# Kernel optimization log

Hardware: AMD Instinct MI355X
Metric: run time of the kernel (lower is better)

## Reference

```python
import jax, jax.numpy as jnp
import numpy as np
from jax import lax

B, T, U, V = 4, 256, 64, 1024   # batch, enc frames, max target len, vocab (blank=0)
F, H, HD, J = 80, 512, 512, 512  # feat dim, enc dim, dec dim, joint dim
NEG = -1e30


def setup_inputs() -> dict:
    key = jax.random.key(0)
    ks = jax.random.split(key, 10)
    inputs = jax.random.normal(ks[0], (B, T, F), dtype=jnp.float32)
    targets = jax.random.randint(ks[1], (B, U), 1, V, dtype=jnp.int32)  # labels exclude blank=0
    input_lengths = jax.random.randint(ks[2], (B,), T // 2, T + 1, dtype=jnp.int32)
    target_lengths = jax.random.randint(ks[3], (B,), U // 2, U + 1, dtype=jnp.int32)
    s = 0.02
    W_enc = jax.random.normal(ks[4], (F, H), dtype=jnp.float32) * s
    emb = jax.random.normal(ks[5], (V, HD), dtype=jnp.float32) * s
    W_jenc = jax.random.normal(ks[6], (H, J), dtype=jnp.float32) * s
    W_jdec = jax.random.normal(ks[7], (HD, J), dtype=jnp.float32) * s
    b_j = jnp.zeros((J,), dtype=jnp.float32)
    W_out = jax.random.normal(ks[8], (J, V), dtype=jnp.float32) * s
    b_out = jnp.zeros((V,), dtype=jnp.float32)
    return {"inputs": inputs, "W_enc": W_enc, "emb": emb, "W_jenc": W_jenc,
            "W_jdec": W_jdec, "b_j": b_j, "W_out": W_out, "b_out": b_out,
            "targets": targets, "input_lengths": input_lengths,
            "target_lengths": target_lengths}


def rnnt_loss(log_probs, targets, in_lens, tgt_lens):
    """RNN-T loss (blank=0, 'gather' variant: gather blank/label lps, then DP).
    log_probs: (B,T,U+1,V) log-softmaxed joint. Returns mean loss over batch."""
    Bq, Tq, U1, _ = log_probs.shape
    Uq = U1 - 1
    blank_lp = log_probs[..., 0]                                    # (B,T,U+1)
    lbl_lp = jnp.take_along_axis(
        log_probs[:, :, :Uq, :],
        jnp.broadcast_to(targets[:, None, :, None], (Bq, Tq, Uq, 1)),
        axis=3)[..., 0]                                             # (B,T,U)
    u_idx = jnp.arange(Uq)
    lbl_lp = jnp.where(u_idx[None, None, :] < tgt_lens[:, None, None], lbl_lp, NEG)

    def row(a, py):
        # a: (B,U+1) = alpha_prev + blank emission; py: (B,U) label lps this frame
        def step(c, x):
            a_u, py_prev = x
            c = jnp.logaddexp(a_u, c + py_prev)
            return c, c
        c0 = a[:, 0]
        _, rest = lax.scan(step, c0, (a[:, 1:].T, py.T))            # (U,B)
        return jnp.concatenate([c0[:, None], rest.T], axis=1)      # (B,U+1)

    # t=0 row: alpha[0,u] = cumsum of label lps at frame 0
    alpha0 = jnp.concatenate(
        [jnp.zeros((Bq, 1), log_probs.dtype),
         jnp.cumsum(lbl_lp[:, 0, :], axis=1)], axis=1)              # (B,U+1)

    def tstep(alpha_prev, x):
        blank_prev, py_t = x
        alpha = row(alpha_prev + blank_prev, py_t)
        return alpha, alpha

    xs = (jnp.swapaxes(blank_lp[:, :-1, :], 0, 1),                  # (T-1,B,U+1)
          jnp.swapaxes(lbl_lp[:, 1:, :], 0, 1))                    # (T-1,B,U)
    _, rest = lax.scan(tstep, alpha0, xs)
    alphas = jnp.concatenate([alpha0[None], rest], axis=0)          # (T,B,U+1)

    b = jnp.arange(Bq)
    t_last = in_lens - 1
    a_fin = alphas[t_last, b, tgt_lens] + blank_lp[b, t_last, tgt_lens]
    return -jnp.mean(a_fin)


def reference(inputs, W_enc, emb, W_jenc, W_jdec, b_j, W_out, b_out,
              targets, input_lengths, target_lengths):
    enc = inputs @ W_enc                                            # (B,T,H) encoder
    padded = jnp.concatenate(
        [jnp.zeros((targets.shape[0], 1), targets.dtype), targets], axis=1)
    dec = emb[padded]                                               # (B,U+1,HD) decoder
    e = enc @ W_jenc                                                # (B,T,J)
    d = dec @ W_jdec                                                # (B,U+1,J)
    h = jnp.tanh(e[:, :, None, :] + d[:, None, :, :] + b_j)        # (B,T,U+1,J)
    logits = h @ W_out + b_out                                      # (B,T,U+1,V)
    log_probs = jax.nn.log_softmax(logits, axis=-1)
    return rnnt_loss(log_probs, targets, input_lengths, target_lengths)
```

## Files before the change

### kernel.cpp

```cpp
#include <hip/hip_runtime.h>
#include <stdint.h>

#define NEGF (-1e30f)

typedef unsigned short ushort_t;
typedef unsigned char uchar_t;
typedef __attribute__((ext_vector_type(2))) long v2i64;
typedef __attribute__((ext_vector_type(4))) float f32x4;

constexpr int cB = 4, cT = 256, cU = 64, cU1 = 65, cV = 1024, cF = 80, cH = 512, cJ = 512;
constexpr int cM = cB * cT * cU1;
constexpr int cTU = cT * cU1;

__device__ __forceinline__ float tanh_fast(float x){
  float t = x * x;
  float num = x * (27.f + t);
  float den = fmaf(9.f, t, 27.f);
  float r = num * __builtin_amdgcn_rcpf(den);
  return fminf(1.f, fmaxf(-1.f, r));
}

__device__ __forceinline__ float logadd(float x, float y){
  float m = fmaxf(x, y);
  return m + __logf(1.f + __expf(-fabsf(x - y)));
}

__device__ __forceinline__ int pk8(float a, float b, float c, float d){
  int v = __builtin_amdgcn_cvt_pk_fp8_f32(a, b, 0, false);
  v = __builtin_amdgcn_cvt_pk_fp8_f32(c, d, v, true);
  return v;
}

__global__ __launch_bounds__(256) void k_pre(
    const float* __restrict__ W_enc, const float* __restrict__ W_jenc,
    float* __restrict__ Wcomb,
    const float* __restrict__ emb, const int* __restrict__ targets,
    const float* __restrict__ W_jdec, const float* __restrict__ b_j,
    float* __restrict__ dmatb,
    const float* __restrict__ W_out, uchar_t* __restrict__ WTf8)
{
  __shared__ float sA[4][512];
  int bid = blockIdx.x;
  int tid = threadIdx.x;

  if (bid < 170){
    bool isW = (bid < 40);
    int id = isW ? bid : bid - 40;
    int bx = id & 1, by = id >> 1;
    int m0 = by * 4;
    int col = bx * 256 + tid;
    const float* Bm = isW ? W_jenc : W_jdec;
    for (int i = tid; i < 4 * 512; i += 256){
      int r = i >> 9, c = i & 511;
      if (isW){
        sA[r][c] = W_enc[(size_t)(m0 + r) * 512 + c];
      } else {
        int row = m0 + r;
        int b = row / cU1, u = row % cU1;
        int src = (u == 0) ? 0 : targets[b * cU + (u - 1)];
        sA[r][c] = emb[(size_t)src * cH + c];
      }
    }
    __syncthreads();
    float a0 = 0.f, a1 = 0.f, a2 = 0.f, a3 = 0.f;
#pragma unroll 8
    for (int k = 0; k < 512; k++){
      float bv = Bm[(size_t)k * cJ + col];
      a0 = fmaf(sA[0][k], bv, a0);
      a1 = fmaf(sA[1][k], bv, a1);
      a2 = fmaf(sA[2][k], bv, a2);
      a3 = fmaf(sA[3][k], bv, a3);
    }
    float bb = isW ? 0.f : b_j[col];
    float* C = isW ? Wcomb : dmatb;
    C[(size_t)(m0 + 0) * cJ + col] = a0 + bb;
    C[(size_t)(m0 + 1) * cJ + col] = a1 + bb;
    C[(size_t)(m0 + 2) * cJ + col] = a2 + bb;
    C[(size_t)(m0 + 3) * cJ + col] = a3 + bb;
  } else {
    int id = bid - 170;
    int bn = id & 3, ksp = id >> 2;
    int lane = tid & 63, nth = tid >> 6;
    int c16 = lane & 15, quad = lane >> 4;
    int jA = ksp * 64 + quad * 8;
#pragma unroll
    for (int i = 0; i < 4; i++){
      int nt16 = nth * 4 + i;
      int n = bn * 256 + nt16 * 16 + c16;
      unsigned int p[4];
#pragma unroll
      for (int h = 0; h < 4; h++){
        int j0 = jA + (h >> 1) * 32 + (h & 1) * 4;
        float w0 = W_out[(size_t)(j0 + 0) * cV + n] * 32.f;
        float w1 = W_out[(size_t)(j0 + 1) * cV + n] * 32.f;
        float w2 = W_out[(size_t)(j0 + 2) * cV + n] * 32.f;
        float w3 = W_out[(size_t)(j0 + 3) * cV + n] * 32.f;
        p[h] = (unsigned)pk8(w0, w1, w2, w3);
      }
      uint4 pack; pack.x = p[0]; pack.y = p[1]; pack.z = p[2]; pack.w = p[3];
      *(uint4*)(WTf8 + (((size_t)(bn * 8 + ksp) * 16 + nt16) * 64 + lane) * 16) = pack;
    }
  }
}

__global__ void k_gemm_e(const float* __restrict__ A, const float* __restrict__ Bm,
                         float* __restrict__ C){
  __shared__ float sA[4][80];
  int m0 = blockIdx.y * 4;
  int col = blockIdx.x * 256 + threadIdx.x;
  for (int i = threadIdx.x; i < 4 * 80; i += 256)
    sA[i / 80][i % 80] = A[(size_t)(m0 + i / 80) * 80 + (i % 80)];
  __syncthreads();
  float a0 = 0.f, a1 = 0.f, a2 = 0.f, a3 = 0.f;
#pragma unroll 8
  for (int k = 0; k < 80; k++){
    float bv = Bm[(size_t)k * cJ + col];
    a0 = fmaf(sA[0][k], bv, a0);
    a1 = fmaf(sA[1][k], bv, a1);
    a2 = fmaf(sA[2][k], bv, a2);
    a3 = fmaf(sA[3][k], bv, a3);
  }
  C[(size_t)(m0 + 0) * cJ + col] = a0;
  C[(size_t)(m0 + 1) * cJ + col] = a1;
  C[(size_t)(m0 + 2) * cJ + col] = a2;
  C[(size_t)(m0 + 3) * cJ + col] = a3;
}

__global__ __launch_bounds__(256) void k_hf(const float* __restrict__ e,
                                            const float* __restrict__ dmatb,
                                            uchar_t* __restrict__ Hbf8){
  __shared__ uchar_t sH[16 * 520];
  int tid = threadIdx.x;
  int wid = tid >> 6, lane = tid & 63;
  int c16 = lane & 15, quad = lane >> 4;
  int bm = blockIdx.x;
  int bu = bm >> 1, thalf = bm & 1;
  int b = bu / cU1;
  int t0 = thalf * 128;

  float dj[8];
  const float4* dp = (const float4*)(dmatb + (size_t)bu * cJ + lane * 8);
  float4 dA = dp[0], dB = dp[1];
  dj[0] = dA.x; dj[1] = dA.y; dj[2] = dA.z; dj[3] = dA.w;
  dj[4] = dB.x; dj[5] = dB.y; dj[6] = dB.z; dj[7] = dB.w;

  const float* erow0 = e + ((size_t)(b * cT + t0)) * cJ + lane * 8;
  uchar_t* outb = Hbf8 + (size_t)bm * 65536 + lane * 16;

  for (int mg = 0; mg < 8; mg++){
#pragma unroll
    for (int rr = 0; rr < 4; rr++){
      int rloc = wid * 4 + rr;
      const float* ep = erow0 + ((size_t)(mg * 16 + rloc)) * cJ;
      float4 e0 = *(const float4*)ep;
      float4 e1 = *(const float4*)(ep + 4);
      int v0 = pk8(tanh_fast(e0.x + dj[0]), tanh_fast(e0.y + dj[1]),
                   tanh_fast(e0.z + dj[2]), tanh_fast(e0.w + dj[3]));
      int v1 = pk8(tanh_fast(e1.x + dj[4]), tanh_fast(e1.y + dj[5]),
                   tanh_fast(e1.z + dj[6]), tanh_fast(e1.w + dj[7]));
      uint2 pk; pk.x = (unsigned)v0; pk.y = (unsigned)v1;
      *(uint2*)(sH + rloc * 520 + lane * 8) = pk;
    }
    __syncthreads();
#pragma unroll
    for (int q = 0; q < 2; q++){
      int ksp = wid * 2 + q;
      uint2 lo = *(const uint2*)(sH + c16 * 520 + ksp * 64 + quad * 8);
      uint2 hi = *(const uint2*)(sH + c16 * 520 + ksp * 64 + 32 + quad * 8);
      uint4 pack; pack.x = lo.x; pack.y = lo.y; pack.z = hi.x; pack.w = hi.y;
      *(uint4*)(outb + ((size_t)ksp * 8 + mg) * 1024) = pack;
    }
    __syncthreads();
  }
}

__global__ __launch_bounds__(256, 3) void k_joint(
    const uchar_t* __restrict__ Hbf8, const uchar_t* __restrict__ WTf8,
    const float* __restrict__ b_out, const int* __restrict__ targets,
    float* __restrict__ ps,
    float* __restrict__ blank_g, float* __restrict__ lbl_g)
{
  __shared__ float redS[2][128];

  int tid = threadIdx.x;
  int wid = tid >> 6, lane = tid & 63;
  int quad = lane >> 4, c16 = lane & 15;
  int wm = wid & 1, wn = wid >> 1;
  int bid = blockIdx.x;
  int bm = ((bid >> 6) << 3) + (bid & 7);
  int bn = (bid >> 3) & 7;
  int bu = bm >> 1, thalf = bm & 1;
  int b = bu / cU1, u = bu - b * cU1;
  int tg = (u < cU) ? targets[b * cU + u] : -1;
  int lin0 = bu * cT + thalf * 128;

  f32x4 acc[4][4];
#pragma unroll
  for (int i = 0; i < 4; i++)
#pragma unroll
    for (int j = 0; j < 4; j++)
      acc[i][j] = (f32x4){0.f, 0.f, 0.f, 0.f};

  const uchar_t* aP = Hbf8 + (size_t)bm * 65536 + (wm * 4) * 1024 + lane * 16;
  const uchar_t* bP = WTf8 + (size_t)(bn >> 1) * 131072 + ((bn & 1) * 8 + wn * 4) * 1024 + lane * 16;

#pragma unroll
  for (int ksp = 0; ksp < 8; ksp++){
    v2i64 af[4], bf[4];
#pragma unroll
    for (int mt = 0; mt < 4; mt++)
      af[mt] = *(const v2i64*)(aP + (size_t)ksp * 8192 + mt * 1024);
#pragma unroll
    for (int nt = 0; nt < 4; nt++)
      bf[nt] = *(const v2i64*)(bP + (size_t)ksp * 16384 + nt * 1024);
#pragma unroll
    for (int h = 0; h < 2; h++)
#pragma unroll
      for (int mt = 0; mt < 4; mt++)
#pragma unroll
        for (int nt = 0; nt < 4; nt++)
          acc[mt][nt] = __builtin_amdgcn_mfma_f32_16x16x32_fp8_fp8(af[mt][h], bf[nt][h], acc[mt][nt], 0, 0, 0);
  }

  float bv[4];
#pragma unroll
  for (int nt = 0; nt < 4; nt++) bv[nt] = b_out[bn * 128 + (wn * 4 + nt) * 16 + c16];

  bool ownL = (tg >= 0) && ((tg >> 7) == bn) && (((tg >> 6) & 1) == wn);
  int ntO = (tg >> 4) & 3;
  int tgc = tg & 15;
  const float descale = 1.f / 32.f;

#pragma unroll
  for (int mt = 0; mt < 4; mt++){
#pragma unroll
    for (int r = 0; r < 4; r++){
      int rl = wm * 64 + mt * 16 + quad * 4 + r;
      float l[4];
#pragma unroll
      for (int nt = 0; nt < 4; nt++) l[nt] = fmaf(acc[mt][nt][r], descale, bv[nt]);
      if (bn == 0 && wn == 0 && c16 == 0) blank_g[lin0 + rl] = l[0];
      if (ownL && c16 == tgc){
        float v = l[0];
#pragma unroll
        for (int k = 1; k < 4; k++) v = (ntO == k) ? l[k] : v;
        lbl_g[lin0 + rl] = v;
      }
      float s = __expf(l[0]) + __expf(l[1]) + __expf(l[2]) + __expf(l[3]);
      s += __shfl_xor(s, 1, 64);
      s += __shfl_xor(s, 2, 64);
      s += __shfl_xor(s, 4, 64);
      s += __shfl_xor(s, 8, 64);
      if (c16 == 0) redS[wn][rl] = s;
    }
  }
  __syncthreads();
  if (tid < 128)
    ps[(size_t)bn * cM + lin0 + tid] = redS[0][tid] + redS[1][tid];
}

__global__ __launch_bounds__(256) void k_lse(
    const float* __restrict__ ps, const float* __restrict__ blank_g,
    const float* __restrict__ lbl_g,
    float* __restrict__ blankd, float* __restrict__ lbld)
{
  int cell = blockIdx.x * 256 + threadIdx.x;
  float S = 0.f;
#pragma unroll
  for (int p = 0; p < 8; p++) S += ps[(size_t)p * cM + cell];
  float lse = __logf(S);
  int u = (cell % cTU) >> 8;
  blankd[cell] = blank_g[cell] - lse;
  lbld[cell] = (u < cU) ? (lbl_g[cell] - lse) : NEGF;
}

__global__ __launch_bounds__(256) void k_dp(
    const float* __restrict__ blankd, const float* __restrict__ lbld,
    const int* __restrict__ in_len, const int* __restrict__ tgt_len,
    float* __restrict__ afin)
{
  __shared__ float sbb[cTU];
  __shared__ float slb[cTU];
  __shared__ float sS[256];
  int b = blockIdx.x;
  int tl  = tgt_len[b];
  size_t base = (size_t)b * cTU;
  for (int i = threadIdx.x; i < cTU / 4; i += 256){
    ((float4*)sbb)[i] = ((const float4*)(blankd + base))[i];
    float4 v = ((const float4*)(lbld + base))[i];
    int row = (i * 4) >> 8;
    if (row >= tl){ v.x = NEGF; v.y = NEGF; v.z = NEGF; v.w = NEGF; }
    ((float4*)slb)[i] = v;
  }
  __syncthreads();
  if (threadIdx.x >= 64) return;

  int u = threadIdx.x;
  int til = in_len[b] - 1;
  bool cap64 = (tl == 64);
  bool isTL = (u == tl);
  const float* pbu  = sbb + (u << 8);
  const float* pbu1 = sbb + (((u >= 1) ? u - 1 : 0) << 8);
  const float* plu1 = slb + (((u >= 1) ? u - 1 : 0) << 8);
  const float* plu2 = slb + (((u >= 2) ? u - 2 : 0) << 8);
  bool u1 = (u >= 1), u2 = (u >= 2);
  float fb = pbu[til];

  float A = (u == 0) ? 0.f : NEGF;
  float res = 0.f;

  auto ld = [&](const float* p, int i, bool ok) -> float {
    bool v = ok & (i >= 0) & (i <= 255);
    int ic = (i < 0) ? 0 : ((i > 255) ? 255 : i);
    float x = p[ic];
    return v ? x : NEGF;
  };

  int i0 = -u;
  float o0 = ld(pbu,  i0,     true);
  float o1 = ld(pbu,  i0 + 1, true);
  float o2 = ld(plu1, i0 + 1, u1);
  float o3 = ld(pbu1, i0 + 1, u1);
  float o4 = ld(plu1, i0 + 2, u1);
  float o5 = ld(plu2, i0 + 2, u2);

  for (int g = 0; g < 159; g++){
    float c0 = o0, c1 = o1, c2 = o2, c3 = o3, c4 = o4, c5 = o5;
    int i0n = i0 + 2;
    o0 = ld(pbu,  i0n,     true);
    o1 = ld(pbu,  i0n + 1, true);
    o2 = ld(plu1, i0n + 1, u1);
    o3 = ld(pbu1, i0n + 1, u1);
    o4 = ld(plu1, i0n + 2, u1);
    o5 = ld(plu2, i0n + 2, u2);

    float up1 = __shfl_up(A, 1, 64);
    float up2 = __shfl_up(A, 2, 64);

    float C0 = c0 + c1;
    float C1 = logadd(c2 + c1, c3 + c4);
    float C2 = c5 + c4;

    bool tv1 = (i0 + 1 >= 0) & (i0 + 1 <= 255);
    float Amid = logadd(A + c0, up1 + c2);
    Amid = tv1 ? Amid : NEGF;
    bool tv2 = (i0 + 2 >= 0) & (i0 + 2 <= 255);
    float Anew = logadd(logadd(A + C0, up1 + C1), up2 + C2);
    Anew = tv2 ? Anew : NEGF;

    if (isTL && (i0 + 1) == til) res = Amid + fb;
    if (isTL && (i0 + 2) == til) res = Anew + fb;
    if (u == 63){
      if (tv1) sS[i0 + 1] = Amid;
      if (tv2) sS[i0 + 2] = Anew;
    }
    A = Anew;
    i0 = i0n;
  }

  if (cap64){
    const float* pb64 = sbb + (64 << 8);
    const float* pl63 = slb + (63 << 8);
    float A64 = sS[0] + pl63[0];
    for (int t = 1; t <= til; t++)
      A64 = logadd(A64 + pb64[t - 1], sS[t] + pl63[t]);
    if (u == 0) res = A64 + pb64[til];
  }

  res += __shfl_xor(res, 1, 64);
  res += __shfl_xor(res, 2, 64);
  res += __shfl_xor(res, 4, 64);
  res += __shfl_xor(res, 8, 64);
  res += __shfl_xor(res, 16, 64);
  res += __shfl_xor(res, 32, 64);
  if (u == 0) afin[b] = res;
}

__global__ void k_final(const float* __restrict__ afin, float* __restrict__ out){
  if (threadIdx.x == 0)
    out[0] = -0.25f * (afin[0] + afin[1] + afin[2] + afin[3]);
}

extern "C" void kernel_launch(void* const* d_in, const int* in_sizes, int n_in,
                              void* d_out, int out_size, void* d_ws, size_t ws_size,
                              hipStream_t stream)
{
  (void)in_sizes; (void)n_in; (void)out_size; (void)ws_size;
  const float* inputs = (const float*)d_in[0];
  const float* W_enc  = (const float*)d_in[1];
  const float* emb    = (const float*)d_in[2];
  const float* W_jenc = (const float*)d_in[3];
  const float* W_jdec = (const float*)d_in[4];
  const float* b_j    = (const float*)d_in[5];
  const float* W_out  = (const float*)d_in[6];
  const float* b_out  = (const float*)d_in[7];
  const int* targets  = (const int*)d_in[8];
  const int* in_len   = (const int*)d_in[9];
  const int* tgt_len  = (const int*)d_in[10];

  char* w = (char*)d_ws;
  auto alloc = [&](size_t bytes){ char* p = w; w += (bytes + 255) & ~(size_t)255; return p; };
  float* Wcomb   = (float*)alloc((size_t)80 * 512 * 4);
  float* e       = (float*)alloc((size_t)1024 * 512 * 4);
  float* dmatb   = (float*)alloc((size_t)260 * 512 * 4);
  float* blank_g = (float*)alloc((size_t)cM * 4);
  float* lbl_g   = (float*)alloc((size_t)cM * 4);
  float* ps      = (float*)alloc((size_t)8 * cM * 4);
  float* blankd  = (float*)alloc((size_t)cM * 4);
  float* lbld    = (float*)alloc((size_t)cM * 4);
  float* afin    = (float*)alloc(256);
  uchar_t* Hbf8  = (uchar_t*)alloc((size_t)520 * 65536);
  uchar_t* WTf8  = (uchar_t*)alloc((size_t)4 * 131072);

  k_pre<<<202, 256, 0, stream>>>(W_enc, W_jenc, Wcomb, emb, targets, W_jdec, b_j, dmatb,
                                 W_out, WTf8);
  k_gemm_e<<<dim3(2, 256), 256, 0, stream>>>(inputs, Wcomb, e);
  k_hf<<<520, 256, 0, stream>>>(e, dmatb, Hbf8);
  k_joint<<<4160, 256, 0, stream>>>(Hbf8, WTf8, b_out, targets, ps, blank_g, lbl_g);
  k_lse<<<260, 256, 0, stream>>>(ps, blank_g, lbl_g, blankd, lbld);
  k_dp<<<4, 256, 0, stream>>>(blankd, lbld, in_len, tgt_len, afin);
  k_final<<<1, 64, 0, stream>>>(afin, (float*)d_out);
}
```

Measured before the change: 244.2 us.

## Switch joint GEMM to 16x16x128 scaled FP8 MFMA with repacked operand layout

```diff
diff --git a/kernel.cpp b/kernel.cpp
--- a/kernel.cpp
+++ b/kernel.cpp
@@ -7,6 +7,7 @@
 typedef unsigned char uchar_t;
 typedef __attribute__((ext_vector_type(2))) long v2i64;
 typedef __attribute__((ext_vector_type(4))) float f32x4;
+typedef __attribute__((ext_vector_type(8))) int v8i32_t;
 
 constexpr int cB = 4, cT = 256, cU = 64, cU1 = 65, cV = 1024, cF = 80, cH = 512, cJ = 512;
 constexpr int cM = cB * cT * cU1;
@@ -79,26 +80,29 @@
     C[(size_t)(m0 + 3) * cJ + col] = a3 + bb;
   } else {
     int id = bid - 170;
-    int bn = id & 3, ksp = id >> 2;
+    int bn4 = id & 3, kq = id >> 2;
     int lane = tid & 63, nth = tid >> 6;
     int c16 = lane & 15, quad = lane >> 4;
-    int jA = ksp * 64 + quad * 8;
+    int jA = kq * 128 + quad * 32;
 #pragma unroll
     for (int i = 0; i < 4; i++){
       int nt16 = nth * 4 + i;
-      int n = bn * 256 + nt16 * 16 + c16;
-      unsigned int p[4];
-#pragma unroll
-      for (int h = 0; h < 4; h++){
-        int j0 = jA + (h >> 1) * 32 + (h & 1) * 4;
+      int n = bn4 * 256 + nt16 * 16 + c16;
+      unsigned int p[8];
+#pragma unroll
+      for (int h = 0; h < 8; h++){
+        int j0 = jA + h * 4;
         float w0 = W_out[(size_t)(j0 + 0) * cV + n] * 32.f;
         float w1 = W_out[(size_t)(j0 + 1) * cV + n] * 32.f;
         float w2 = W_out[(size_t)(j0 + 2) * cV + n] * 32.f;
         float w3 = W_out[(size_t)(j0 + 3) * cV + n] * 32.f;
         p[h] = (unsigned)pk8(w0, w1, w2, w3);
       }
-      uint4 pack; pack.x = p[0]; pack.y = p[1]; pack.z = p[2]; pack.w = p[3];
-      *(uint4*)(WTf8 + (((size_t)(bn * 8 + ksp) * 16 + nt16) * 64 + lane) * 16) = pack;
+      uchar_t* dst = WTf8 + (size_t)bn4 * 131072 + (((size_t)kq * 16 + nt16) * 64 + lane) * 32;
+      uint4 lo; lo.x = p[0]; lo.y = p[1]; lo.z = p[2]; lo.w = p[3];
+      uint4 hi; hi.x = p[4]; hi.y = p[5]; hi.z = p[6]; hi.w = p[7];
+      *(uint4*)dst = lo;
+      *(uint4*)(dst + 16) = hi;
     }
   }
 }
@@ -145,7 +149,7 @@
   dj[4] = dB.x; dj[5] = dB.y; dj[6] = dB.z; dj[7] = dB.w;
 
   const float* erow0 = e + ((size_t)(b * cT + t0)) * cJ + lane * 8;
-  uchar_t* outb = Hbf8 + (size_t)bm * 65536 + lane * 16;
+  uchar_t* outb = Hbf8 + (size_t)bm * 65536 + lane * 32;
 
   for (int mg = 0; mg < 8; mg++){
 #pragma unroll
@@ -162,13 +166,17 @@
       *(uint2*)(sH + rloc * 520 + lane * 8) = pk;
     }
     __syncthreads();
-#pragma unroll
-    for (int q = 0; q < 2; q++){
-      int ksp = wid * 2 + q;
-      uint2 lo = *(const uint2*)(sH + c16 * 520 + ksp * 64 + quad * 8);
-      uint2 hi = *(const uint2*)(sH + c16 * 520 + ksp * 64 + 32 + quad * 8);
-      uint4 pack; pack.x = lo.x; pack.y = lo.y; pack.z = hi.x; pack.w = hi.y;
-      *(uint4*)(outb + ((size_t)ksp * 8 + mg) * 1024) = pack;
+    {
+      const uchar_t* src = sH + c16 * 520 + wid * 128 + quad * 32;
+      uint2 q0 = *(const uint2*)(src + 0);
+      uint2 q1 = *(const uint2*)(src + 8);
+      uint2 q2 = *(const uint2*)(src + 16);
+      uint2 q3 = *(const uint2*)(src + 24);
+      uchar_t* dst = outb + (((size_t)wid * 8 + mg) * 64) * 32;
+      uint4 lo; lo.x = q0.x; lo.y = q0.y; lo.z = q1.x; lo.w = q1.y;
+      uint4 hi; hi.x = q2.x; hi.y = q2.y; hi.z = q3.x; hi.w = q3.y;
+      *(uint4*)dst = lo;
+      *(uint4*)(dst + 16) = hi;
     }
     __syncthreads();
   }
@@ -201,25 +209,24 @@
     for (int j = 0; j < 4; j++)
       acc[i][j] = (f32x4){0.f, 0.f, 0.f, 0.f};
 
-  const uchar_t* aP = Hbf8 + (size_t)bm * 65536 + (wm * 4) * 1024 + lane * 16;
-  const uchar_t* bP = WTf8 + (size_t)(bn >> 1) * 131072 + ((bn & 1) * 8 + wn * 4) * 1024 + lane * 16;
-
-#pragma unroll
-  for (int ksp = 0; ksp < 8; ksp++){
-    v2i64 af[4], bf[4];
+  const uchar_t* aP = Hbf8 + (size_t)bm * 65536 + ((size_t)(wm * 4) * 64 + lane) * 32;
+  const uchar_t* bP = WTf8 + (size_t)(bn >> 1) * 131072 + ((size_t)((bn & 1) * 8 + wn * 4) * 64 + lane) * 32;
+
+#pragma unroll
+  for (int kq = 0; kq < 4; kq++){
+    v8i32_t af[4], bf[4];
 #pragma unroll
     for (int mt = 0; mt < 4; mt++)
-      af[mt] = *(const v2i64*)(aP + (size_t)ksp * 8192 + mt * 1024);
+      af[mt] = *(const v8i32_t*)(aP + (size_t)kq * 16384 + mt * 2048);
 #pragma unroll
     for (int nt = 0; nt < 4; nt++)
-      bf[nt] = *(const v2i64*)(bP + (size_t)ksp * 16384 + nt * 1024);
-#pragma unroll
-    for (int h = 0; h < 2; h++)
-#pragma unroll
-      for (int mt = 0; mt < 4; mt++)
-#pragma unroll
-        for (int nt = 0; nt < 4; nt++)
-          acc[mt][nt] = __builtin_amdgcn_mfma_f32_16x16x32_fp8_fp8(af[mt][h], bf[nt][h], acc[mt][nt], 0, 0, 0);
+      bf[nt] = *(const v8i32_t*)(bP + (size_t)kq * 32768 + nt * 2048);
+#pragma unroll
+    for (int mt = 0; mt < 4; mt++)
+#pragma unroll
+      for (int nt = 0; nt < 4; nt++)
+        acc[mt][nt] = __builtin_amdgcn_mfma_scale_f32_16x16x128_f8f6f4(
+            af[mt], bf[nt], acc[mt][nt], 0, 0, 0, 0x7F7F7F7F, 0, 0x7F7F7F7F);
   }
 
   float bv[4];
@@ -412,7 +419,7 @@
   uchar_t* Hbf8  = (uchar_t*)alloc((size_t)520 * 65536);
   uchar_t* WTf8  = (uchar_t*)alloc((size_t)4 * 131072);
 
-  k_pre<<<202, 256, 0, stream>>>(W_enc, W_jenc, Wcomb, emb, targets, W_jdec, b_j, dmatb,
+  k_pre<<<186, 256, 0, stream>>>(W_enc, W_jenc, Wcomb, emb, targets, W_jdec, b_j, dmatb,
                                  W_out, WTf8);
   k_gemm_e<<<dim3(2, 256), 256, 0, stream>>>(inputs, Wcomb, e);
   k_hf<<<520, 256, 0, stream>>>(e, dmatb, Hbf8);
```

After: 464.8 us. 90.4% more time.

## Replace per-column-block partial sums with atomic accumulation and fold LSE into DP

Applied to the files above, without the earlier changes.

```diff
diff --git a/kernel.cpp b/kernel.cpp
--- a/kernel.cpp
+++ b/kernel.cpp
@@ -37,7 +37,8 @@
     const float* __restrict__ emb, const int* __restrict__ targets,
     const float* __restrict__ W_jdec, const float* __restrict__ b_j,
     float* __restrict__ dmatb,
-    const float* __restrict__ W_out, uchar_t* __restrict__ WTf8)
+    const float* __restrict__ W_out, uchar_t* __restrict__ WTf8,
+    float* __restrict__ S)
 {
   __shared__ float sA[4][512];
   int bid = blockIdx.x;
@@ -77,7 +78,7 @@
     C[(size_t)(m0 + 1) * cJ + col] = a1 + bb;
     C[(size_t)(m0 + 2) * cJ + col] = a2 + bb;
     C[(size_t)(m0 + 3) * cJ + col] = a3 + bb;
-  } else {
+  } else if (bid < 202){
     int id = bid - 170;
     int bn = id & 3, ksp = id >> 2;
     int lane = tid & 63, nth = tid >> 6;
@@ -100,6 +101,10 @@
       uint4 pack; pack.x = p[0]; pack.y = p[1]; pack.z = p[2]; pack.w = p[3];
       *(uint4*)(WTf8 + (((size_t)(bn * 8 + ksp) * 16 + nt16) * 64 + lane) * 16) = pack;
     }
+  } else {
+    int i = (bid - 202) * 1024 + tid * 4;
+    float4 z; z.x = 0.f; z.y = 0.f; z.z = 0.f; z.w = 0.f;
+    *(float4*)(S + i) = z;
   }
 }
 
@@ -177,7 +182,7 @@
 __global__ __launch_bounds__(256, 3) void k_joint(
     const uchar_t* __restrict__ Hbf8, const uchar_t* __restrict__ WTf8,
     const float* __restrict__ b_out, const int* __restrict__ targets,
-    float* __restrict__ ps,
+    float* __restrict__ S,
     float* __restrict__ blank_g, float* __restrict__ lbl_g)
 {
   __shared__ float redS[2][128];
@@ -256,26 +261,12 @@
   }
   __syncthreads();
   if (tid < 128)
-    ps[(size_t)bn * cM + lin0 + tid] = redS[0][tid] + redS[1][tid];
-}
-
-__global__ __launch_bounds__(256) void k_lse(
-    const float* __restrict__ ps, const float* __restrict__ blank_g,
-    const float* __restrict__ lbl_g,
-    float* __restrict__ blankd, float* __restrict__ lbld)
-{
-  int cell = blockIdx.x * 256 + threadIdx.x;
-  float S = 0.f;
-#pragma unroll
-  for (int p = 0; p < 8; p++) S += ps[(size_t)p * cM + cell];
-  float lse = __logf(S);
-  int u = (cell % cTU) >> 8;
-  blankd[cell] = blank_g[cell] - lse;
-  lbld[cell] = (u < cU) ? (lbl_g[cell] - lse) : NEGF;
+    atomicAdd(&S[lin0 + tid], redS[0][tid] + redS[1][tid]);
 }
 
 __global__ __launch_bounds__(256) void k_dp(
-    const float* __restrict__ blankd, const float* __restrict__ lbld,
+    const float* __restrict__ blank_g, const float* __restrict__ lbl_g,
+    const float* __restrict__ S,
     const int* __restrict__ in_len, const int* __restrict__ tgt_len,
     float* __restrict__ afin)
 {
@@ -286,11 +277,19 @@
   int tl  = tgt_len[b];
   size_t base = (size_t)b * cTU;
   for (int i = threadIdx.x; i < cTU / 4; i += 256){
-    ((float4*)sbb)[i] = ((const float4*)(blankd + base))[i];
-    float4 v = ((const float4*)(lbld + base))[i];
+    float4 bg = ((const float4*)(blank_g + base))[i];
+    float4 lg = ((const float4*)(lbl_g + base))[i];
+    float4 sv = ((const float4*)(S + base))[i];
+    float4 ls;
+    ls.x = __logf(sv.x); ls.y = __logf(sv.y); ls.z = __logf(sv.z); ls.w = __logf(sv.w);
+    float4 ob;
+    ob.x = bg.x - ls.x; ob.y = bg.y - ls.y; ob.z = bg.z - ls.z; ob.w = bg.w - ls.w;
+    ((float4*)sbb)[i] = ob;
     int row = (i * 4) >> 8;
-    if (row >= tl){ v.x = NEGF; v.y = NEGF; v.z = NEGF; v.w = NEGF; }
-    ((float4*)slb)[i] = v;
+    float4 ol;
+    if (row >= tl){ ol.x = NEGF; ol.y = NEGF; ol.z = NEGF; ol.w = NEGF; }
+    else { ol.x = lg.x - ls.x; ol.y = lg.y - ls.y; ol.z = lg.z - ls.z; ol.w = lg.w - ls.w; }
+    ((float4*)slb)[i] = ol;
   }
   __syncthreads();
   if (threadIdx.x >= 64) return;
@@ -405,19 +404,16 @@
   float* dmatb   = (float*)alloc((size_t)260 * 512 * 4);
   float* blank_g = (float*)alloc((size_t)cM * 4);
   float* lbl_g   = (float*)alloc((size_t)cM * 4);
-  float* ps      = (float*)alloc((size_t)8 * cM * 4);
-  float* blankd  = (float*)alloc((size_t)cM * 4);
-  float* lbld    = (float*)alloc((size_t)cM * 4);
+  float* S       = (float*)alloc((size_t)cM * 4);
   float* afin    = (float*)alloc(256);
   uchar_t* Hbf8  = (uchar_t*)alloc((size_t)520 * 65536);
   uchar_t* WTf8  = (uchar_t*)alloc((size_t)4 * 131072);
 
-  k_pre<<<202, 256, 0, stream>>>(W_enc, W_jenc, Wcomb, emb, targets, W_jdec, b_j, dmatb,
-                                 W_out, WTf8);
+  k_pre<<<267, 256, 0, stream>>>(W_enc, W_jenc, Wcomb, emb, targets, W_jdec, b_j, dmatb,
+                                 W_out, WTf8, S);
   k_gemm_e<<<dim3(2, 256), 256, 0, stream>>>(inputs, Wcomb, e);
   k_hf<<<520, 256, 0, stream>>>(e, dmatb, Hbf8);
-  k_joint<<<4160, 256, 0, stream>>>(Hbf8, WTf8, b_out, targets, ps, blank_g, lbl_g);
-  k_lse<<<260, 256, 0, stream>>>(ps, blank_g, lbl_g, blankd, lbld);
-  k_dp<<<4, 256, 0, stream>>>(blankd, lbld, in_len, tgt_len, afin);
+  k_joint<<<4160, 256, 0, stream>>>(Hbf8, WTf8, b_out, targets, S, blank_g, lbl_g);
+  k_dp<<<4, 256, 0, stream>>>(blank_g, lbl_g, S, in_len, tgt_len, afin);
   k_final<<<1, 64, 0, stream>>>(afin, (float*)d_out);
 }
```

Measured after the change: 246.7 us. Within noise of the previous version (+1.0%).
